# Performance work log

Hardware: AMD Instinct MI355X
Metric: run time of the kernel (lower is better)

Reference implementation:

```python
import jax, jax.numpy as jnp
import numpy as np

B, N, D, NS, ITERS = 32, 2048, 512, 8, 3
EPS = 1e-8
SCALE = D ** -0.5
LN_EPS = 1e-5


def _ln(x, g, b):
    m = x.mean(-1, keepdims=True)
    v = ((x - m) ** 2).mean(-1, keepdims=True)
    return (x - m) * jax.lax.rsqrt(v + LN_EPS) * g + b


def setup_inputs() -> dict:
    key = jax.random.key(0)
    ks = iter(jax.random.split(key, 40))
    w = lambda *s: jax.random.normal(next(ks), s, jnp.float32) * 0.02
    inp = {
        'inputs': jax.random.normal(next(ks), (B, N, D), jnp.float32),
        'slot_noise': jax.random.normal(next(ks), (B, NS, D), jnp.float32),
        'slots_mu': jax.random.normal(next(ks), (1, 1, D), jnp.float32),
        'slots_logsigma': w(1, 1, D),
        'k_w': w(D, D), 'k_b': jnp.zeros((D,), jnp.float32),
        'v_w': w(D, D), 'v_b': jnp.zeros((D,), jnp.float32),
        'gru_w_ih': w(3 * D, D), 'gru_w_hh': w(3 * D, D),
        'gru_b_ih': jnp.zeros((3 * D,), jnp.float32),
        'gru_b_hh': jnp.zeros((3 * D,), jnp.float32),
        'ln_in_g': jnp.ones((D,), jnp.float32), 'ln_in_b': jnp.zeros((D,), jnp.float32),
        'ln_slots_g': jnp.ones((D,), jnp.float32), 'ln_slots_b': jnp.zeros((D,), jnp.float32),
        'ln_pre_g': jnp.ones((D,), jnp.float32), 'ln_pre_b': jnp.zeros((D,), jnp.float32),
        'mlp1_w': w(1024, D), 'mlp1_b': jnp.zeros((1024,), jnp.float32),
        'mlp2_w': w(1024, 1024), 'mlp2_b': jnp.zeros((1024,), jnp.float32),
        'mlp3_w': w(512, 1024), 'mlp3_b': jnp.zeros((512,), jnp.float32),
        'mlp4_w': w(256, 512), 'mlp4_b': jnp.zeros((256,), jnp.float32),
    }
    return inp


def reference(inputs, slot_noise, slots_mu, slots_logsigma, k_w, k_b, v_w, v_b,
              gru_w_ih, gru_w_hh, gru_b_ih, gru_b_hh,
              ln_in_g, ln_in_b, ln_slots_g, ln_slots_b, ln_pre_g, ln_pre_b,
              mlp1_w, mlp1_b, mlp2_w, mlp2_b, mlp3_w, mlp3_b, mlp4_w, mlp4_b):
    b, n, d = inputs.shape
    # stochastic slot init: mu + exp(logsigma) * noise  -> [b, ns, d]
    slots = slots_mu + jnp.exp(slots_logsigma) * slot_noise
    x = _ln(inputs, ln_in_g, ln_in_b)
    k = x @ k_w.T + k_b
    v = x @ v_w.T + v_b
    updates = slots
    for _ in range(ITERS):
        slots_prev = slots
        q = _ln(slots, ln_slots_g, ln_slots_b)
        dots = jnp.einsum('bid,bjd->bij', q, k) * SCALE  # [b, ns, n]
        attn = jax.nn.softmax(dots, axis=1) + EPS        # softmax over slot axis
        attn = attn / attn.sum(-1, keepdims=True)        # renorm over tokens
        updates = jnp.einsum('bjd,bij->bid', v, attn)    # [b, ns, d]
        # GRUCell(updates, slots_prev), then residual add of updates
        u = updates.reshape(-1, d)
        h = slots_prev.reshape(-1, d)
        gi = u @ gru_w_ih.T + gru_b_ih
        gh = h @ gru_w_hh.T + gru_b_hh
        i_r, i_z, i_n = jnp.split(gi, 3, axis=-1)
        h_r, h_z, h_n = jnp.split(gh, 3, axis=-1)
        r = jax.nn.sigmoid(i_r + h_r)
        z = jax.nn.sigmoid(i_z + h_z)
        nn_ = jnp.tanh(i_n + r * h_n)
        h_new = (1.0 - z) * nn_ + z * h
        slots = (u + h_new).reshape(b, -1, d)
    # output MLP with exact GELU (torch default)
    s = _ln(slots, ln_pre_g, ln_pre_b)
    s = jax.nn.gelu(s @ mlp1_w.T + mlp1_b, approximate=False)
    s = jax.nn.gelu(s @ mlp2_w.T + mlp2_b, approximate=False)
    s = jax.nn.gelu(s @ mlp3_w.T + mlp3_b, approximate=False)
    s = s @ mlp4_w.T + mlp4_b
    return (updates, s)
```

## Files before the change

### kernel.cpp

```cpp
#include <hip/hip_runtime.h>
#include <math.h>

#define Bb 32
#define Nn 2048
#define Dd 512
#define NS 8
#define ITERS 3
#define EPSf 1e-8f
#define SCALEf 0.04419417382415922f
#define LN_EPSf 1e-5f

#define QHS 520
#define PTS 136
#define CHUNKS 16

typedef _Float16 half8 __attribute__((ext_vector_type(8)));
typedef float f32x4 __attribute__((ext_vector_type(4)));

__device__ __forceinline__ float waveReduceSum(float v) {
    #pragma unroll
    for (int m = 32; m >= 1; m >>= 1) v += __shfl_xor(v, m);
    return v;
}

__device__ __forceinline__ float gelu_exact(float x) {
    return 0.5f * x * (1.0f + erff(x * 0.7071067811865476f));
}

__device__ __forceinline__ void async_copy16(const _Float16* g, _Float16* l) {
    __builtin_amdgcn_global_load_lds(
        (const __attribute__((address_space(1))) unsigned int*)g,
        (__attribute__((address_space(3))) unsigned int*)l, 16, 0, 0);
}

__global__ __launch_bounds__(256) void megapack_kernel(
    const float* __restrict__ k_w, const float* __restrict__ v_w,
    const float* __restrict__ w_ih, const float* __restrict__ w_hh,
    const float* __restrict__ m1, const float* __restrict__ m2,
    const float* __restrict__ m3, const float* __restrict__ m4,
    _Float16* __restrict__ Bkv, _Float16* __restrict__ Bih, _Float16* __restrict__ Bhh,
    _Float16* __restrict__ Bm1, _Float16* __restrict__ Bm2,
    _Float16* __restrict__ Bm3, _Float16* __restrict__ Bm4) {
    int bid = blockIdx.x, tid = threadIdx.x;
    const float* src; _Float16* dst; int kbits, base;
    if (bid < 2048) {
        int i = bid * 256 + tid;
        Bkv[i] = (_Float16)(i < 262144 ? k_w[i] : v_w[i - 262144]);
        return;
    }
    else if (bid < 5120)  { src = w_ih; dst = Bih; kbits = 9;  base = 2048; }
    else if (bid < 8192)  { src = w_hh; dst = Bhh; kbits = 9;  base = 5120; }
    else if (bid < 10240) { src = m1;   dst = Bm1; kbits = 9;  base = 8192; }
    else if (bid < 14336) { src = m2;   dst = Bm2; kbits = 10; base = 10240; }
    else if (bid < 16384) { src = m3;   dst = Bm3; kbits = 10; base = 14336; }
    else                  { src = m4;   dst = Bm4; kbits = 9;  base = 16384; }
    int e = (bid - base) * 256 + tid;
    int K = 1 << kbits;
    int row = e >> kbits, k = e & (K - 1);
    _Float16 h = (_Float16)src[e];
    _Float16* d = dst + ((size_t)row << (kbits + 1));
    d[k] = h;
    d[K + k] = h;
}

__global__ __launch_bounds__(256) void pack_ln_single_kernel(
    const float* __restrict__ x, const float* __restrict__ g, const float* __restrict__ b,
    _Float16* __restrict__ Ap) {
    int wid = blockIdx.x * 4 + (threadIdx.x >> 6);
    int lane = threadIdx.x & 63;
    const float4* row4 = (const float4*)(x + (size_t)wid * Dd);
    float4 va = row4[lane * 2], vb = row4[lane * 2 + 1];
    float v[8] = {va.x, va.y, va.z, va.w, vb.x, vb.y, vb.z, vb.w};
    float s = 0.f, sq = 0.f;
    #pragma unroll
    for (int t = 0; t < 8; ++t) { s += v[t]; sq += v[t] * v[t]; }
    s = waveReduceSum(s);
    sq = waveReduceSum(sq);
    float m = s * (1.0f / Dd);
    float var = sq * (1.0f / Dd) - m * m;
    float rs = rsqrtf(var + LN_EPSf);
    const float4* g4 = (const float4*)g;
    const float4* b4 = (const float4*)b;
    float4 ga = g4[lane * 2], gb = g4[lane * 2 + 1];
    float4 ba = b4[lane * 2], bb = b4[lane * 2 + 1];
    float gg[8] = {ga.x, ga.y, ga.z, ga.w, gb.x, gb.y, gb.z, gb.w};
    float bbv[8] = {ba.x, ba.y, ba.z, ba.w, bb.x, bb.y, bb.z, bb.w};
    half8 o;
    #pragma unroll
    for (int t = 0; t < 8; ++t) o[t] = (_Float16)((v[t] - m) * rs * gg[t] + bbv[t]);
    *(half8*)(Ap + (size_t)wid * Dd + lane * 8) = o;
}

__global__ __launch_bounds__(256) void slots_init_kernel(
    const float* __restrict__ noise, const float* __restrict__ mu,
    const float* __restrict__ ls, float* __restrict__ slots, _Float16* __restrict__ A2,
    const float* __restrict__ lns_g, const float* __restrict__ lns_b,
    _Float16* __restrict__ qh) {
    int row = blockIdx.x * 4 + (threadIdx.x >> 6);
    int lane = threadIdx.x & 63;
    float val[8];
    float s = 0.f, sq = 0.f;
    #pragma unroll
    for (int t = 0; t < 8; ++t) {
        int d = t * 64 + lane;
        float v = mu[d] + expf(ls[d]) * noise[(size_t)row * 512 + d];
        val[t] = v;
        s += v; sq += v * v;
        slots[(size_t)row * 512 + d] = v;
        _Float16 hi = (_Float16)v;
        A2[(size_t)(256 + row) * 1024 + d] = hi;
        A2[(size_t)(256 + row) * 1024 + 512 + d] = (_Float16)(v - (float)hi);
    }
    s = waveReduceSum(s);
    sq = waveReduceSum(sq);
    float m = s * (1.0f / Dd);
    float var = sq * (1.0f / Dd) - m * m;
    float rs = rsqrtf(var + LN_EPSf);
    #pragma unroll
    for (int t = 0; t < 8; ++t) {
        int d = t * 64 + lane;
        qh[(size_t)row * 512 + d] = (_Float16)(((val[t] - m) * rs * lns_g[d] + lns_b[d]) * SCALEf);
    }
}

__global__ __launch_bounds__(256) void kv_hgemm_kernel(
    const _Float16* __restrict__ Apack, const _Float16* __restrict__ Bkv,
    const float* __restrict__ k_b, const float* __restrict__ v_b,
    _Float16* __restrict__ khalf, _Float16* __restrict__ vT) {
    __shared__ _Float16 smem[17408];
    _Float16* As = smem;
    _Float16* Bs = smem + 8192;
    const int f = blockIdx.x;
    const int m0 = ((f & 7) + ((f >> 6) << 3)) * 128;
    const int n0 = ((f >> 3) & 7) * 128;
    const int tid = threadIdx.x;
    const int w = tid >> 6, lane = tid & 63;
    const int r8 = lane >> 3, seg = lane & 7;
    const int lr = lane & 15, quad = lane >> 4;
    const int wm = w >> 1, wn = w & 1;
    f32x4 acc[4][4];
    #pragma unroll
    for (int i = 0; i < 4; ++i)
        #pragma unroll
        for (int j = 0; j < 4; ++j) acc[i][j] = (f32x4){0.f, 0.f, 0.f, 0.f};
    for (int k0 = 0; k0 < 512; k0 += 64) {
        __syncthreads();
        #pragma unroll
        for (int g = 0; g < 4; ++g) {
            int grp = w * 4 + g;
            int row = grp * 8 + r8;
            async_copy16(Apack + (size_t)(m0 + row) * 512 + k0 + seg * 8, As + grp * 512);
            async_copy16(Bkv + (size_t)(n0 + row) * 512 + k0 + seg * 8, Bs + grp * 512);
        }
        __syncthreads();
        #pragma unroll
        for (int kk = 0; kk < 2; ++kk) {
            half8 a[4], b[4];
            #pragma unroll
            for (int t = 0; t < 4; ++t) {
                a[t] = *(const half8*)(As + (wm * 64 + t * 16 + lr) * 64 + kk * 32 + quad * 8);
                b[t] = *(const half8*)(Bs + (wn * 64 + t * 16 + lr) * 64 + kk * 32 + quad * 8);
            }
            #pragma unroll
            for (int mt = 0; mt < 4; ++mt)
                #pragma unroll
                for (int nt = 0; nt < 4; ++nt)
                    acc[mt][nt] = __builtin_amdgcn_mfma_f32_16x16x32_f16(
                        a[mt], b[nt], acc[mt][nt], 0, 0, 0);
        }
    }
    __syncthreads();
    const bool isK = (n0 < 512);
    #pragma unroll
    for (int mt = 0; mt < 4; ++mt)
        #pragma unroll
        for (int nt = 0; nt < 4; ++nt) {
            int ml = wm * 64 + mt * 16 + quad * 4;
            int nl = wn * 64 + nt * 16 + lr;
            float bv = isK ? k_b[n0 + nl] : v_b[n0 - 512 + nl];
            #pragma unroll
            for (int r = 0; r < 4; ++r) {
                _Float16 h = (_Float16)(acc[mt][nt][r] + bv);
                if (isK) smem[(ml + r) * 136 + nl] = h;
                else     smem[nl * 136 + ml + r] = h;
            }
        }
    __syncthreads();
    int r = tid >> 1, half = tid & 1;
    _Float16* dst;
    if (isK) {
        dst = khalf + (size_t)(m0 + r) * 512 + n0 + half * 64;
    } else {
        int b = m0 >> 11, j0 = m0 & 2047, d0 = n0 - 512;
        dst = vT + ((size_t)b * 512 + d0 + r) * 2048 + j0 + half * 64;
    }
    #pragma unroll
    for (int c = 0; c < 8; ++c)
        *(half8*)(dst + c * 8) = *(const half8*)(smem + r * 136 + half * 64 + c * 8);
}

__global__ __launch_bounds__(256) void attn_kernel(
    const _Float16* __restrict__ qh_g,
    const _Float16* __restrict__ khalf, const _Float16* __restrict__ vT,
    float* __restrict__ rawp, float* __restrict__ sumsp) {
    const int b = blockIdx.y, chunk = blockIdx.x;
    __shared__ _Float16 qh[16 * QHS];
    __shared__ _Float16 pT[16 * PTS];
    __shared__ float sums_lds[64];
    const int tid = threadIdx.x, w = tid >> 6, lane = tid & 63;
    const int lr = lane & 15, quad = lane >> 4;

    {
        int r = tid >> 5;
        int c = (tid & 31) * 16;
        *(half8*)(qh + r * QHS + c) = *(const half8*)(qh_g + ((size_t)b * NS + r) * 512 + c);
        *(half8*)(qh + r * QHS + c + 8) = *(const half8*)(qh_g + ((size_t)b * NS + r) * 512 + c + 8);
        half8 z = {};
        *(half8*)(qh + (8 + r) * QHS + c) = z;
        *(half8*)(qh + (8 + r) * QHS + c + 8) = z;
    }
    __syncthreads();

    const int j0 = chunk * 128 + w * 32;
    f32x4 dots[2];
    dots[0] = (f32x4){0.f, 0.f, 0.f, 0.f};
    dots[1] = (f32x4){0.f, 0.f, 0.f, 0.f};
    for (int ks = 0; ks < 16; ++ks) {
        half8 bq = *(const half8*)(qh + lr * QHS + ks * 32 + quad * 8);
        #pragma unroll
        for (int mf = 0; mf < 2; ++mf) {
            half8 ak = *(const half8*)(khalf + ((size_t)b * Nn + j0 + mf * 16 + lr) * 512 + ks * 32 + quad * 8);
            dots[mf] = __builtin_amdgcn_mfma_f32_16x16x32_f16(ak, bq, dots[mf], 0, 0, 0);
        }
    }
    float ssum = 0.f;
    #pragma unroll
    for (int mf = 0; mf < 2; ++mf) {
        f32x4 d = dots[mf];
        f32x4 mx = d;
        #pragma unroll
        for (int msk = 1; msk <= 4; msk <<= 1) {
            #pragma unroll
            for (int r = 0; r < 4; ++r) mx[r] = fmaxf(mx[r], __shfl_xor(mx[r], msk));
        }
        f32x4 p;
        #pragma unroll
        for (int r = 0; r < 4; ++r) p[r] = __expf(d[r] - mx[r]);
        f32x4 sm = p;
        #pragma unroll
        for (int msk = 1; msk <= 4; msk <<= 1) {
            #pragma unroll
            for (int r = 0; r < 4; ++r) sm[r] += __shfl_xor(sm[r], msk);
        }
        #pragma unroll
        for (int r = 0; r < 4; ++r) {
            _Float16 ph = (_Float16)(p[r] / sm[r] + EPSf);
            pT[lr * PTS + w * 32 + mf * 16 + quad * 4 + r] = ph;
            ssum += (float)ph;
        }
    }
    ssum += __shfl_xor(ssum, 16);
    ssum += __shfl_xor(ssum, 32);
    if (lane < 16) sums_lds[w * 16 + lane] = ssum;
    __syncthreads();

    f32x4 acc[8];
    #pragma unroll
    for (int nf = 0; nf < 8; ++nf) acc[nf] = (f32x4){0.f, 0.f, 0.f, 0.f};
    #pragma unroll
    for (int kc = 0; kc < 4; ++kc) {
        half8 ap = *(const half8*)(pT + lr * PTS + kc * 32 + quad * 8);
        #pragma unroll
        for (int nf = 0; nf < 8; ++nf) {
            int dcol = w * 128 + nf * 16 + lr;
            half8 bv = *(const half8*)(vT + ((size_t)b * 512 + dcol) * 2048 + chunk * 128 + kc * 32 + quad * 8);
            acc[nf] = __builtin_amdgcn_mfma_f32_16x16x32_f16(ap, bv, acc[nf], 0, 0, 0);
        }
    }
    if (quad < 2) {
        #pragma unroll
        for (int nf = 0; nf < 8; ++nf) {
            #pragma unroll
            for (int r = 0; r < 4; ++r) {
                int slot = quad * 4 + r;
                rawp[(((size_t)chunk * Bb + b) * NS + slot) * Dd + w * 128 + nf * 16 + lr] = acc[nf][r];
            }
        }
    }
    if (w == 0 && lane < NS) {
        float tot = sums_lds[lane] + sums_lds[16 + lane] + sums_lds[32 + lane] + sums_lds[48 + lane];
        sumsp[((size_t)chunk * Bb + b) * NS + lane] = tot;
    }
}

__global__ __launch_bounds__(256) void finalize_kernel(
    const float* __restrict__ rawp, const float* __restrict__ sumsp,
    float* __restrict__ u, float* __restrict__ out0, _Float16* __restrict__ A2) {
    int idx = blockIdx.x * 256 + threadIdx.x;
    int row = idx >> 9, k = idx & 511;
    float rs = 0.f, ss = 0.f;
    #pragma unroll
    for (int c = 0; c < CHUNKS; ++c) {
        rs += rawp[(size_t)c * 131072 + idx];
        ss += sumsp[c * 256 + row];
    }
    float val = rs / ss;
    u[idx] = val;
    out0[idx] = val;
    _Float16 hi = (_Float16)val;
    A2[(size_t)row * 1024 + k] = hi;
    A2[(size_t)row * 1024 + 512 + k] = (_Float16)(val - (float)hi);
}

__device__ __forceinline__ void hgemm64_core(
    const _Float16* __restrict__ A, const _Float16* __restrict__ Bw,
    int K2, f32x4 acc[2][2], _Float16* As, _Float16* Bs) {
    const int tid = threadIdx.x;
    const int w = tid >> 6, lane = tid & 63;
    const int r8 = lane >> 3, seg = lane & 7;
    const int lr = lane & 15, quad = lane >> 4;
    const int wm = w >> 1, wn = w & 1;
    for (int k0 = 0; k0 < K2; k0 += 64) {
        __syncthreads();
        #pragma unroll
        for (int p = 0; p < 2; ++p) {
            int grp = p * 4 + w;
            int row = grp * 8 + r8;
            async_copy16(A + (size_t)row * K2 + k0 + seg * 8, As + grp * 512);
            async_copy16(Bw + (size_t)row * K2 + k0 + seg * 8, Bs + grp * 512);
        }
        __syncthreads();
        #pragma unroll
        for (int kk = 0; kk < 2; ++kk) {
            half8 a[2], b[2];
            #pragma unroll
            for (int t = 0; t < 2; ++t) {
                a[t] = *(const half8*)(As + (wm * 32 + t * 16 + lr) * 64 + kk * 32 + quad * 8);
                b[t] = *(const half8*)(Bs + (wn * 32 + t * 16 + lr) * 64 + kk * 32 + quad * 8);
            }
            #pragma unroll
            for (int mt = 0; mt < 2; ++mt)
                #pragma unroll
                for (int nt = 0; nt < 2; ++nt)
                    acc[mt][nt] = __builtin_amdgcn_mfma_f32_16x16x32_f16(
                        a[mt], b[nt], acc[mt][nt], 0, 0, 0);
        }
    }
}

template <int ACT, int PACK>
__global__ __launch_bounds__(256) void hgemm64_kernel(
    const _Float16* __restrict__ A, const _Float16* __restrict__ Bw,
    const float* __restrict__ bias, float* __restrict__ C, _Float16* __restrict__ P,
    int K2, int N, int Kp) {
    __shared__ _Float16 As[4096], Bs[4096];
    const int m0 = blockIdx.y * 64, n0 = blockIdx.x * 64;
    f32x4 acc[2][2];
    #pragma unroll
    for (int i = 0; i < 2; ++i)
        #pragma unroll
        for (int j = 0; j < 2; ++j) acc[i][j] = (f32x4){0.f, 0.f, 0.f, 0.f};
    hgemm64_core(A + (size_t)m0 * K2, Bw + (size_t)n0 * K2, K2, acc, As, Bs);
    const int tid = threadIdx.x;
    const int w = tid >> 6, lane = tid & 63;
    const int lr = lane & 15, quad = lane >> 4;
    const int wm = w >> 1, wn = w & 1;
    #pragma unroll
    for (int mt = 0; mt < 2; ++mt)
        #pragma unroll
        for (int nt = 0; nt < 2; ++nt) {
            int n = n0 + wn * 32 + nt * 16 + lr;
            float bv = bias[n];
            #pragma unroll
            for (int r = 0; r < 4; ++r) {
                int m = m0 + wm * 32 + mt * 16 + quad * 4 + r;
                float val = acc[mt][nt][r] + bv;
                if (ACT) val = gelu_exact(val);
                if (PACK) {
                    _Float16 hi = (_Float16)val;
                    P[(size_t)m * 2 * Kp + n] = hi;
                    P[(size_t)m * 2 * Kp + Kp + n] = (_Float16)(val - (float)hi);
                } else {
                    C[(size_t)m * N + n] = val;
                }
            }
        }
}

__global__ __launch_bounds__(256) void gru_gemm_kernel(
    const _Float16* __restrict__ A2, const _Float16* __restrict__ Bih,
    const _Float16* __restrict__ Bhh, const float* __restrict__ b_ih,
    const float* __restrict__ b_hh, float* __restrict__ gi, float* __restrict__ gh) {
    __shared__ _Float16 As[4096], Bs[4096];
    const int by = blockIdx.y;
    const int n0 = blockIdx.x * 64;
    const _Float16* Ap; const _Float16* Bw; const float* bias; float* C;
    if (by < 4) { Ap = A2 + (size_t)by * 64 * 1024;        Bw = Bih; bias = b_ih; C = gi + (size_t)by * 64 * 1536; }
    else        { Ap = A2 + (size_t)(256 + (by - 4) * 64) * 1024; Bw = Bhh; bias = b_hh; C = gh + (size_t)(by - 4) * 64 * 1536; }
    f32x4 acc[2][2];
    #pragma unroll
    for (int i = 0; i < 2; ++i)
        #pragma unroll
        for (int j = 0; j < 2; ++j) acc[i][j] = (f32x4){0.f, 0.f, 0.f, 0.f};
    hgemm64_core(Ap, Bw + (size_t)n0 * 1024, 1024, acc, As, Bs);
    const int tid = threadIdx.x;
    const int w = tid >> 6, lane = tid & 63;
    const int lr = lane & 15, quad = lane >> 4;
    const int wm = w >> 1, wn = w & 1;
    #pragma unroll
    for (int mt = 0; mt < 2; ++mt)
        #pragma unroll
        for (int nt = 0; nt < 2; ++nt) {
            int n = n0 + wn * 32 + nt * 16 + lr;
            float bv = bias[n];
            #pragma unroll
            for (int r = 0; r < 4; ++r) {
                int m = wm * 32 + mt * 16 + quad * 4 + r;
                C[(size_t)m * 1536 + n] = acc[mt][nt][r] + bv;
            }
        }
}

__global__ __launch_bounds__(256) void gru_elem_kernel(
    const float* __restrict__ gi, const float* __restrict__ gh,
    const float* __restrict__ u, float* __restrict__ slots, _Float16* __restrict__ A2,
    const float* __restrict__ lns_g, const float* __restrict__ lns_b,
    _Float16* __restrict__ qh,
    const float* __restrict__ lnp_g, const float* __restrict__ lnp_b,
    _Float16* __restrict__ P1, int last) {
    int row = blockIdx.x * 4 + (threadIdx.x >> 6);
    int lane = threadIdx.x & 63;
    const float* gir = gi + (size_t)row * 1536;
    const float* ghr = gh + (size_t)row * 1536;
    float val[8];
    #pragma unroll
    for (int t = 0; t < 8; ++t) {
        int d = t * 64 + lane;
        float ir = gir[d], iz = gir[512 + d], in_ = gir[1024 + d];
        float hr = ghr[d], hz = ghr[512 + d], hn = ghr[1024 + d];
        float r = 1.0f / (1.0f + expf(-(ir + hr)));
        float z = 1.0f / (1.0f + expf(-(iz + hz)));
        float n = tanhf(in_ + r * hn);
        float h = slots[(size_t)row * 512 + d];
        float hnew = (1.0f - z) * n + z * h;
        float vv = u[(size_t)row * 512 + d] + hnew;
        val[t] = vv;
        slots[(size_t)row * 512 + d] = vv;
        _Float16 hi = (_Float16)vv;
        A2[(size_t)(256 + row) * 1024 + d] = hi;
        A2[(size_t)(256 + row) * 1024 + 512 + d] = (_Float16)(vv - (float)hi);
    }
    float s = 0.f, sq = 0.f;
    #pragma unroll
    for (int t = 0; t < 8; ++t) { s += val[t]; sq += val[t] * val[t]; }
    s = waveReduceSum(s);
    sq = waveReduceSum(sq);
    float m = s * (1.0f / Dd);
    float var = sq * (1.0f / Dd) - m * m;
    float rs = rsqrtf(var + LN_EPSf);
    if (!last) {
        #pragma unroll
        for (int t = 0; t < 8; ++t) {
            int d = t * 64 + lane;
            qh[(size_t)row * 512 + d] =
                (_Float16)(((val[t] - m) * rs * lns_g[d] + lns_b[d]) * SCALEf);
        }
    } else {
        #pragma unroll
        for (int t = 0; t < 8; ++t) {
            int d = t * 64 + lane;
            float a = (val[t] - m) * rs * lnp_g[d] + lnp_b[d];
            _Float16 hi = (_Float16)a;
            P1[(size_t)row * 1024 + d] = hi;
            P1[(size_t)row * 1024 + 512 + d] = (_Float16)(a - (float)hi);
        }
    }
}

extern "C" void kernel_launch(void* const* d_in, const int* in_sizes, int n_in,
                              void* d_out, int out_size, void* d_ws, size_t ws_size,
                              hipStream_t stream) {
    const float* inputs   = (const float*)d_in[0];
    const float* noise    = (const float*)d_in[1];
    const float* mu       = (const float*)d_in[2];
    const float* lsig     = (const float*)d_in[3];
    const float* k_w      = (const float*)d_in[4];
    const float* k_b      = (const float*)d_in[5];
    const float* v_w      = (const float*)d_in[6];
    const float* v_b      = (const float*)d_in[7];
    const float* w_ih     = (const float*)d_in[8];
    const float* w_hh     = (const float*)d_in[9];
    const float* b_ih     = (const float*)d_in[10];
    const float* b_hh     = (const float*)d_in[11];
    const float* ln_in_g  = (const float*)d_in[12];
    const float* ln_in_b  = (const float*)d_in[13];
    const float* ln_s_g   = (const float*)d_in[14];
    const float* ln_s_b   = (const float*)d_in[15];
    const float* ln_p_g   = (const float*)d_in[16];
    const float* ln_p_b   = (const float*)d_in[17];
    const float* mlp1_w   = (const float*)d_in[18];
    const float* mlp1_b   = (const float*)d_in[19];
    const float* mlp2_w   = (const float*)d_in[20];
    const float* mlp2_b   = (const float*)d_in[21];
    const float* mlp3_w   = (const float*)d_in[22];
    const float* mlp3_b   = (const float*)d_in[23];
    const float* mlp4_w   = (const float*)d_in[24];
    const float* mlp4_b   = (const float*)d_in[25];
    float* out0 = (float*)d_out;
    float* out1 = (float*)d_out + Bb * NS * Dd;

    char* wp = (char*)d_ws;
    auto alloc = [&](size_t bytes) -> void* {
        void* p = (void*)wp;
        wp += (bytes + 255) & ~(size_t)255;
        return p;
    };
    const size_t MR = (size_t)Bb * Nn;
    _Float16* Apack = (_Float16*)alloc(MR * 512 * 2);
    _Float16* khalf = (_Float16*)alloc(MR * 512 * 2);
    _Float16* vT    = (_Float16*)alloc((size_t)Bb * 512 * Nn * 2);
    _Float16* Bkv   = (_Float16*)alloc((size_t)1024 * 512 * 2);
    _Float16* Bih   = (_Float16*)alloc((size_t)1536 * 1024 * 2);
    _Float16* Bhh   = (_Float16*)alloc((size_t)1536 * 1024 * 2);
    _Float16* Bm1   = (_Float16*)alloc((size_t)1024 * 1024 * 2);
    _Float16* Bm2   = (_Float16*)alloc((size_t)1024 * 2048 * 2);
    _Float16* Bm3   = (_Float16*)alloc((size_t)512 * 2048 * 2);
    _Float16* Bm4   = (_Float16*)alloc((size_t)256 * 1024 * 2);
    float* slots    = (float*)alloc((size_t)Bb * NS * Dd * 4);
    _Float16* qh    = (_Float16*)alloc((size_t)Bb * NS * Dd * 2);
    float* rawp     = (float*)alloc((size_t)CHUNKS * Bb * NS * Dd * 4);
    float* sumsp    = (float*)alloc((size_t)CHUNKS * Bb * NS * 4);
    float* ubuf     = (float*)alloc((size_t)Bb * NS * Dd * 4);
    float* gi       = (float*)alloc((size_t)Bb * NS * 1536 * 4);
    float* gh       = (float*)alloc((size_t)Bb * NS * 1536 * 4);
    _Float16* A2    = (_Float16*)alloc((size_t)512 * 1024 * 2);
    _Float16* P1    = (_Float16*)alloc((size_t)256 * 1024 * 2);
    _Float16* P2    = (_Float16*)alloc((size_t)256 * 2048 * 2);
    _Float16* P3    = (_Float16*)alloc((size_t)256 * 2048 * 2);
    _Float16* P4    = (_Float16*)alloc((size_t)256 * 1024 * 2);

    megapack_kernel<<<16896, 256, 0, stream>>>(
        k_w, v_w, w_ih, w_hh, mlp1_w, mlp2_w, mlp3_w, mlp4_w,
        Bkv, Bih, Bhh, Bm1, Bm2, Bm3, Bm4);
    pack_ln_single_kernel<<<MR / 4, 256, 0, stream>>>(inputs, ln_in_g, ln_in_b, Apack);
    slots_init_kernel<<<64, 256, 0, stream>>>(noise, mu, lsig, slots, A2, ln_s_g, ln_s_b, qh);

    kv_hgemm_kernel<<<4096, 256, 0, stream>>>(Apack, Bkv, k_b, v_b, khalf, vT);

    for (int it = 0; it < ITERS; ++it) {
        attn_kernel<<<dim3(CHUNKS, Bb), 256, 0, stream>>>(qh, khalf, vT, rawp, sumsp);
        finalize_kernel<<<512, 256, 0, stream>>>(rawp, sumsp, ubuf, out0, A2);
        gru_gemm_kernel<<<dim3(24, 8), 256, 0, stream>>>(A2, Bih, Bhh, b_ih, b_hh, gi, gh);
        gru_elem_kernel<<<64, 256, 0, stream>>>(gi, gh, ubuf, slots, A2,
                                                ln_s_g, ln_s_b, qh,
                                                ln_p_g, ln_p_b, P1, it == ITERS - 1 ? 1 : 0);
    }

    hgemm64_kernel<1, 1><<<dim3(16, 4), 256, 0, stream>>>(P1, Bm1, mlp1_b, nullptr, P2, 1024, 1024, 1024);
    hgemm64_kernel<1, 1><<<dim3(16, 4), 256, 0, stream>>>(P2, Bm2, mlp2_b, nullptr, P3, 2048, 1024, 1024);
    hgemm64_kernel<1, 1><<<dim3(8, 4), 256, 0, stream>>>(P3, Bm3, mlp3_b, nullptr, P4, 2048, 512, 512);
    hgemm64_kernel<0, 0><<<dim3(4, 4), 256, 0, stream>>>(P4, Bm4, mlp4_b, out1, nullptr, 1024, 256, 256);
}
```

Baseline: 652.6 us.

## Split attention into smaller token chunks and drop LDS staging in KV GEMM

The attention kernel now processes 64 tokens per block instead of 128, doubling CHUNKS to 32 so that twice as many blocks run per batch, which raises parallelism across the GPU. The KV projection GEMM stops staging A and B tiles through LDS with async copies and barriers, and instead loads MFMA fragments directly from global memory. This removes the synchronisation cost but relies on cache hits for data reuse. More chunks also mean more partial results that the downstream reduction must combine.

```diff
diff --git a/kernel.cpp b/kernel.cpp
--- a/kernel.cpp
+++ b/kernel.cpp
@@ -11,8 +11,8 @@
 #define LN_EPSf 1e-5f
 
 #define QHS 520
-#define PTS 136
-#define CHUNKS 16
+#define PTS 72
+#define CHUNKS 32
 
 typedef _Float16 half8 __attribute__((ext_vector_type(8)));
 typedef float f32x4 __attribute__((ext_vector_type(4)));
@@ -128,14 +128,11 @@
     const float* __restrict__ k_b, const float* __restrict__ v_b,
     _Float16* __restrict__ khalf, _Float16* __restrict__ vT) {
     __shared__ _Float16 smem[17408];
-    _Float16* As = smem;
-    _Float16* Bs = smem + 8192;
     const int f = blockIdx.x;
     const int m0 = ((f & 7) + ((f >> 6) << 3)) * 128;
     const int n0 = ((f >> 3) & 7) * 128;
     const int tid = threadIdx.x;
     const int w = tid >> 6, lane = tid & 63;
-    const int r8 = lane >> 3, seg = lane & 7;
     const int lr = lane & 15, quad = lane >> 4;
     const int wm = w >> 1, wn = w & 1;
     f32x4 acc[4][4];
@@ -143,33 +140,25 @@
     for (int i = 0; i < 4; ++i)
         #pragma unroll
         for (int j = 0; j < 4; ++j) acc[i][j] = (f32x4){0.f, 0.f, 0.f, 0.f};
-    for (int k0 = 0; k0 < 512; k0 += 64) {
-        __syncthreads();
-        #pragma unroll
-        for (int g = 0; g < 4; ++g) {
-            int grp = w * 4 + g;
-            int row = grp * 8 + r8;
-            async_copy16(Apack + (size_t)(m0 + row) * 512 + k0 + seg * 8, As + grp * 512);
-            async_copy16(Bkv + (size_t)(n0 + row) * 512 + k0 + seg * 8, Bs + grp * 512);
-        }
-        __syncthreads();
-        #pragma unroll
-        for (int kk = 0; kk < 2; ++kk) {
-            half8 a[4], b[4];
-            #pragma unroll
-            for (int t = 0; t < 4; ++t) {
-                a[t] = *(const half8*)(As + (wm * 64 + t * 16 + lr) * 64 + kk * 32 + quad * 8);
-                b[t] = *(const half8*)(Bs + (wn * 64 + t * 16 + lr) * 64 + kk * 32 + quad * 8);
-            }
-            #pragma unroll
-            for (int mt = 0; mt < 4; ++mt)
-                #pragma unroll
-                for (int nt = 0; nt < 4; ++nt)
-                    acc[mt][nt] = __builtin_amdgcn_mfma_f32_16x16x32_f16(
-                        a[mt], b[nt], acc[mt][nt], 0, 0, 0);
-        }
-    }
-    __syncthreads();
+
+    const _Float16* Abase = Apack + (size_t)(m0 + wm * 64 + lr) * 512 + quad * 8;
+    const _Float16* Bbase = Bkv + (size_t)(n0 + wn * 64 + lr) * 512 + quad * 8;
+    #pragma unroll 2
+    for (int ks = 0; ks < 16; ++ks) {
+        half8 a[4], b[4];
+        #pragma unroll
+        for (int t = 0; t < 4; ++t) {
+            a[t] = *(const half8*)(Abase + (size_t)t * 16 * 512 + ks * 32);
+            b[t] = *(const half8*)(Bbase + (size_t)t * 16 * 512 + ks * 32);
+        }
+        #pragma unroll
+        for (int mt = 0; mt < 4; ++mt)
+            #pragma unroll
+            for (int nt = 0; nt < 4; ++nt)
+                acc[mt][nt] = __builtin_amdgcn_mfma_f32_16x16x32_f16(
+                    a[mt], b[nt], acc[mt][nt], 0, 0, 0);
+    }
+
     const bool isK = (n0 < 512);
     #pragma unroll
     for (int mt = 0; mt < 4; ++mt)
@@ -221,22 +210,16 @@
     }
     __syncthreads();
 
-    const int j0 = chunk * 128 + w * 32;
-    f32x4 dots[2];
-    dots[0] = (f32x4){0.f, 0.f, 0.f, 0.f};
-    dots[1] = (f32x4){0.f, 0.f, 0.f, 0.f};
+    const int j0 = chunk * 64 + w * 16;
+    f32x4 dots = (f32x4){0.f, 0.f, 0.f, 0.f};
     for (int ks = 0; ks < 16; ++ks) {
         half8 bq = *(const half8*)(qh + lr * QHS + ks * 32 + quad * 8);
-        #pragma unroll
-        for (int mf = 0; mf < 2; ++mf) {
-            half8 ak = *(const half8*)(khalf + ((size_t)b * Nn + j0 + mf * 16 + lr) * 512 + ks * 32 + quad * 8);
-            dots[mf] = __builtin_amdgcn_mfma_f32_16x16x32_f16(ak, bq, dots[mf], 0, 0, 0);
-        }
+        half8 ak = *(const half8*)(khalf + ((size_t)b * Nn + j0 + lr) * 512 + ks * 32 + quad * 8);
+        dots = __builtin_amdgcn_mfma_f32_16x16x32_f16(ak, bq, dots, 0, 0, 0);
     }
     float ssum = 0.f;
-    #pragma unroll
-    for (int mf = 0; mf < 2; ++mf) {
-        f32x4 d = dots[mf];
+    {
+        f32x4 d = dots;
         f32x4 mx = d;
         #pragma unroll
         for (int msk = 1; msk <= 4; msk <<= 1) {
@@ -255,7 +238,7 @@
         #pragma unroll
         for (int r = 0; r < 4; ++r) {
             _Float16 ph = (_Float16)(p[r] / sm[r] + EPSf);
-            pT[lr * PTS + w * 32 + mf * 16 + quad * 4 + r] = ph;
+            pT[lr * PTS + w * 16 + quad * 4 + r] = ph;
             ssum += (float)ph;
         }
     }
@@ -268,12 +251,12 @@
     #pragma unroll
     for (int nf = 0; nf < 8; ++nf) acc[nf] = (f32x4){0.f, 0.f, 0.f, 0.f};
     #pragma unroll
-    for (int kc = 0; kc < 4; ++kc) {
+    for (int kc = 0; kc < 2; ++kc) {
         half8 ap = *(const half8*)(pT + lr * PTS + kc * 32 + quad * 8);
         #pragma unroll
         for (int nf = 0; nf < 8; ++nf) {
             int dcol = w * 128 + nf * 16 + lr;
-            half8 bv = *(const half8*)(vT + ((size_t)b * 512 + dcol) * 2048 + chunk * 128 + kc * 32 + quad * 8);
+            half8 bv = *(const half8*)(vT + ((size_t)b * 512 + dcol) * 2048 + chunk * 64 + kc * 32 + quad * 8);
             acc[nf] = __builtin_amdgcn_mfma_f32_16x16x32_f16(ap, bv, acc[nf], 0, 0, 0);
         }
     }
```

Result: slower. 811.4 us (+24.3%).
